# Optimization experiments

Hardware: AMD Instinct MI355X
Metric: run time of the kernel (lower is better)

Reference implementation:

```python
import jax, jax.numpy as jnp
import numpy as np

N = 50000       # nodes
E = 800000      # edges (avg degree 16)
D_IN = 128      # input_dim
H = 256         # hidden_dim
Z = H // 2      # 128, latent / conv3-4 width
D_OUT = 64      # output_dim


def _glorot(key, shape):
    fan_in, fan_out = shape
    lim = float(np.sqrt(6.0 / (fan_in + fan_out)))
    return jax.random.uniform(key, shape, jnp.float32, -lim, lim)


def setup_inputs() -> dict:
    key = jax.random.key(0)
    ks = jax.random.split(key, 16)
    inp = {
        "x": jax.random.uniform(ks[0], (N, D_IN), jnp.float32),
        "edge_index": jax.random.randint(ks[1], (2, E), 0, N, jnp.int32),
        "epsilon": jax.random.normal(ks[2], (N, Z), jnp.float32),
        # SAGEConv params: Wl (neighbor/aggr path, with bias), Wr (root path, no bias)
        "Wl1": _glorot(ks[3], (D_IN, H)), "bl1": jnp.zeros((H,), jnp.float32), "Wr1": _glorot(ks[4], (D_IN, H)),
        "Wl2": _glorot(ks[5], (H, H)),    "bl2": jnp.zeros((H,), jnp.float32), "Wr2": _glorot(ks[6], (H, H)),
        "Wl3": _glorot(ks[7], (Z, Z)),    "bl3": jnp.zeros((Z,), jnp.float32), "Wr3": _glorot(ks[8], (Z, Z)),
        "Wl4": _glorot(ks[9], (Z, Z)),    "bl4": jnp.zeros((Z,), jnp.float32), "Wr4": _glorot(ks[10], (Z, Z)),
        "W_lin": _glorot(ks[11], (Z, D_OUT)), "b_lin": jnp.zeros((D_OUT,), jnp.float32),
    }
    return inp


def _sage_conv(x, src, dst, Wl, bl, Wr):
    # PyG SAGEConv (mean aggr): out = lin_l(mean_{j in N(i)} x_j) + lin_r(x_i)
    msg = x[src]                                             # [E, d] gather
    agg = jax.ops.segment_sum(msg, dst, num_segments=N)      # [N, d]
    cnt = jax.ops.segment_sum(jnp.ones((src.shape[0],), x.dtype), dst, num_segments=N)
    mean = agg / jnp.maximum(cnt, 1.0)[:, None]
    return mean @ Wl + bl + x @ Wr


def reference(x, edge_index, epsilon,
              Wl1, bl1, Wr1, Wl2, bl2, Wr2,
              Wl3, bl3, Wr3, Wl4, bl4, Wr4,
              W_lin, b_lin):
    src, dst = edge_index[0], edge_index[1]
    h = x / 1000.0 - 0.5
    h = jnp.sin(_sage_conv(h, src, dst, Wl1, bl1, Wr1))      # [N, H]
    h = _sage_conv(h, src, dst, Wl2, bl2, Wr2)               # [N, H]
    mean = h[:, :Z]
    log_var = h[:, Z:]
    z = mean + jnp.exp(log_var) * epsilon                    # reparameterize
    h = jax.nn.relu(_sage_conv(z, src, dst, Wl3, bl3, Wr3))
    h = jax.nn.relu(_sage_conv(h, src, dst, Wl4, bl4, Wr4))
    out = jax.nn.sigmoid(h @ W_lin + b_lin) * 1000.0
    return out, mean, log_var
```

## Files before the change

kernel.cpp:

```cpp
#include <hip/hip_runtime.h>
#include <hip/hip_bf16.h>

#define N_NODES 50000
#define E_EDGES 800000

using u16 = unsigned short;
typedef short bf8 __attribute__((ext_vector_type(8)));
typedef float f32x4 __attribute__((ext_vector_type(4)));

__device__ __forceinline__ float bf2f(u16 h) {
    union { unsigned u; float f; } v;
    v.u = ((unsigned)h) << 16;
    return v.f;
}
__device__ __forceinline__ u16 f2bf(float f) {
    union { float f; unsigned u; } v;
    v.f = f;
    unsigned r = v.u + 0x7FFF + ((v.u >> 16) & 1);
    return (u16)(r >> 16);
}

struct WtArgs {
    const float* src[9];
    u16* dst[9];
    int K[9];
    int N[9];
};

__global__ __launch_bounds__(256) void k_wt(WtArgs a) {
    int wi = blockIdx.y;
    int K = a.K[wi], Nn = a.N[wi];
    int tot = K * Nn;
    for (int i = blockIdx.x * 256 + threadIdx.x; i < tot; i += gridDim.x * 256) {
        int n = i / K, k = i % K;
        a.dst[wi][i] = f2bf(a.src[wi][(size_t)k * Nn + n]);
    }
}

__global__ __launch_bounds__(256) void k_prep(const float* __restrict__ x,
                                              u16* __restrict__ h0) {
    int total = N_NODES * 128 / 4;
    for (int i = blockIdx.x * 256 + threadIdx.x; i < total;
         i += gridDim.x * 256) {
        float4 v = *(const float4*)(x + (size_t)i * 4);
        ushort4 o;
        o.x = f2bf(v.x * 0.001f - 0.5f);
        o.y = f2bf(v.y * 0.001f - 0.5f);
        o.z = f2bf(v.z * 0.001f - 0.5f);
        o.w = f2bf(v.w * 0.001f - 0.5f);
        *(ushort4*)(h0 + (size_t)i * 4) = o;
    }
}

__global__ void k_count(const int* __restrict__ dst, int* __restrict__ deg) {
    for (int i = blockIdx.x * blockDim.x + threadIdx.x; i < E_EDGES;
         i += gridDim.x * blockDim.x)
        atomicAdd(&deg[dst[i]], 1);
}

#define SCAN_B 49

__global__ __launch_bounds__(1024) void k_scan1(const int* __restrict__ deg,
                                                int* __restrict__ bsum) {
    __shared__ int sm[1024];
    int i = blockIdx.x * 1024 + threadIdx.x;
    sm[threadIdx.x] = (i < N_NODES) ? deg[i] : 0;
    __syncthreads();
    for (int ofs = 512; ofs > 0; ofs >>= 1) {
        if (threadIdx.x < ofs) sm[threadIdx.x] += sm[threadIdx.x + ofs];
        __syncthreads();
    }
    if (threadIdx.x == 0) bsum[blockIdx.x] = sm[0];
}

__global__ void k_scan2(const int* __restrict__ bsum, int* __restrict__ bofs) {
    int l = threadIdx.x;
    int v = (l < SCAN_B) ? bsum[l] : 0;
    int orig = v;
    for (int d = 1; d < 64; d <<= 1) {
        int u = __shfl_up(v, d, 64);
        if (l >= d) v += u;
    }
    if (l < SCAN_B) bofs[l] = v - orig;
}

__global__ __launch_bounds__(1024) void k_scan3(const int* __restrict__ deg,
                                                const int* __restrict__ bofs,
                                                int* __restrict__ rowptr,
                                                float* __restrict__ dinv) {
    __shared__ int sm[1024];
    int i = blockIdx.x * 1024 + threadIdx.x;
    int d = (i < N_NODES) ? deg[i] : 0;
    sm[threadIdx.x] = d;
    __syncthreads();
    for (int ofs = 1; ofs < 1024; ofs <<= 1) {
        int u = (threadIdx.x >= (unsigned)ofs) ? sm[threadIdx.x - ofs] : 0;
        __syncthreads();
        sm[threadIdx.x] += u;
        __syncthreads();
    }
    if (i < N_NODES) {
        int incl = sm[threadIdx.x] + bofs[blockIdx.x];
        rowptr[i] = incl - d;
        dinv[i] = 1.0f / fmaxf((float)d, 1.0f);
        if (i == N_NODES - 1) rowptr[N_NODES] = incl;
    }
}

__global__ void k_fill(const int* __restrict__ src, const int* __restrict__ dst,
                       const int* __restrict__ rowptr, int* __restrict__ cursor,
                       int* __restrict__ colidx) {
    for (int i = blockIdx.x * blockDim.x + threadIdx.x; i < E_EDGES;
         i += gridDim.x * blockDim.x) {
        int d = dst[i];
        int pos = rowptr[d] + atomicAdd(&cursor[d], 1);
        colidx[pos] = src[i];
    }
}

template <int D>
__global__ __launch_bounds__(256) void k_aggregate(
    const u16* __restrict__ h, const int* __restrict__ rowptr,
    const int* __restrict__ colidx, const float* __restrict__ dinv,
    u16* __restrict__ mean) {
    constexpr int VA = D / 16;
    int node = (int)((blockIdx.x * 256 + threadIdx.x) >> 6);
    int lane = threadIdx.x & 63;
    if (node >= N_NODES) return;
    int sub = lane >> 4, lr = lane & 15;
    int beg = rowptr[node], end = rowptr[node + 1];
    float acc[VA] = {};
    int e = beg + sub;
    for (; e + 4 < end; e += 8) {
        int s0 = colidx[e];
        int s1 = colidx[e + 4];
        const u16* p0 = h + (size_t)s0 * D + lr * VA;
        const u16* p1 = h + (size_t)s1 * D + lr * VA;
        bf8 r0 = *(const bf8*)p0;
        bf8 r1 = *(const bf8*)p1;
        if (VA == 16) {
            bf8 r0b = *(const bf8*)(p0 + 8);
            bf8 r1b = *(const bf8*)(p1 + 8);
#pragma unroll
            for (int j = 0; j < 8; ++j) {
                acc[j] += bf2f((u16)r0[j]) + bf2f((u16)r1[j]);
                acc[8 + j] += bf2f((u16)r0b[j]) + bf2f((u16)r1b[j]);
            }
        } else {
#pragma unroll
            for (int j = 0; j < 8; ++j)
                acc[j] += bf2f((u16)r0[j]) + bf2f((u16)r1[j]);
        }
    }
    for (; e < end; e += 4) {
        int s = colidx[e];
        const u16* row = h + (size_t)s * D + lr * VA;
        bf8 r0 = *(const bf8*)row;
#pragma unroll
        for (int j = 0; j < 8; ++j) acc[j] += bf2f((u16)r0[j]);
        if (VA == 16) {
            bf8 r1 = *(const bf8*)(row + 8);
#pragma unroll
            for (int j = 0; j < 8; ++j) acc[8 + j] += bf2f((u16)r1[j]);
        }
    }
#pragma unroll
    for (int j = 0; j < VA; ++j) {
        acc[j] += __shfl_xor(acc[j], 16);
        acc[j] += __shfl_xor(acc[j], 32);
    }
    if (sub == 0) {
        float inv = dinv[node];
        u16 outv[VA];
#pragma unroll
        for (int j = 0; j < VA; ++j) outv[j] = f2bf(acc[j] * inv);
        u16* o = mean + (size_t)node * D + lr * VA;
        *(bf8*)o = *(bf8*)&outv[0];
        if (VA == 16) *(bf8*)(o + 8) = *(bf8*)&outv[8];
    }
}

enum { ACT_NONE = 0, ACT_SIN = 1, ACT_RELU = 2, ACT_SIGMOID1000 = 3, ACT_VAE = 4 };

template <int K, int NCB, int NC, int ACT, bool OUT_F32, bool TWO_PASS>
__global__ __launch_bounds__(512) void k_gemm(
    const u16* __restrict__ A1, const u16* __restrict__ Wt1,
    const u16* __restrict__ A2, const u16* __restrict__ Wt2,
    const float* __restrict__ bias, void* __restrict__ Cout,
    float* __restrict__ out_mean, float* __restrict__ out_lv,
    const float* __restrict__ eps) {
    constexpr int PK = K + 8;
    constexpr int M = N_NODES;
    constexpr int CH = K / 8;
    constexpr int NG = NCB / 16;
    constexpr int KS = K / 32;
    constexpr int GX = (M / 16 + 7) / 8;
    constexpr int NWG = ((GX + 1) / 2) * 2 * 2;
    constexpr int CPX = NWG / 8;
    extern __shared__ char smem[];
    u16* Bs = (u16*)smem;

    const int bid = blockIdx.x;
    const int wid = (bid & 7) * CPX + (bid >> 3);
    const int x = wid >> 1;
    const int y = wid & 1;
    if (x >= GX) return;

    const int t = threadIdx.x;
    const int lane = t & 63;
    const int wave = t >> 6;
    const int lr = lane & 15;
    const int sub = lane >> 4;
    const int row0 = (x * 8 + wave) * 16;
    const int arow = row0 + lr;
    const bool rowOK = arow < M;

    auto mapRow = [&](int r) {
        if (ACT == ACT_VAE)
            return r < NCB / 2 ? y * (NCB / 2) + r
                               : NC / 2 + y * (NCB / 2) + (r - NCB / 2);
        return y * NCB + r;
    };

    bf8 aF1[KS], aF2[TWO_PASS ? KS : 1];
    {
        const u16* ap = A1 + (size_t)arow * K + sub * 8;
#pragma unroll
        for (int ks = 0; ks < KS; ++ks) {
            bf8 a = {0, 0, 0, 0, 0, 0, 0, 0};
            if (rowOK) a = *(const bf8*)(ap + ks * 32);
            aF1[ks] = a;
        }
    }
    if (TWO_PASS) {
        const u16* ap = A2 + (size_t)arow * K + sub * 8;
#pragma unroll
        for (int ks = 0; ks < KS; ++ks) {
            bf8 a = {0, 0, 0, 0, 0, 0, 0, 0};
            if (rowOK) a = *(const bf8*)(ap + ks * 32);
            aF2[ks] = a;
        }
    }

    f32x4 acc[NG];
#pragma unroll
    for (int i = 0; i < NG; ++i) acc[i] = (f32x4){0.f, 0.f, 0.f, 0.f};

    auto stageW = [&](const u16* __restrict__ Wt) {
#pragma unroll
        for (int i = 0; i < NCB * CH / 512; ++i) {
            int c = t + i * 512;
            int r = c / CH, kc = c % CH;
            *(bf8*)&Bs[r * PK + kc * 8] =
                *(const bf8*)(Wt + (size_t)mapRow(r) * K + kc * 8);
        }
    };
    auto mm = [&](const bf8* aF) {
#pragma unroll
        for (int ks = 0; ks < KS; ++ks) {
#pragma unroll
            for (int ni = 0; ni < NG; ++ni) {
                bf8 b = *(const bf8*)&Bs[(ni * 16 + lr) * PK + ks * 32 + sub * 8];
                acc[ni] =
                    __builtin_amdgcn_mfma_f32_16x16x32_bf16(aF[ks], b, acc[ni],
                                                            0, 0, 0);
            }
        }
    };

    stageW(Wt1);
    __syncthreads();
    mm(aF1);
    if (TWO_PASS) {
        __syncthreads();
        stageW(Wt2);
        __syncthreads();
        mm(aF2);
    }

    if (ACT == ACT_VAE) {
#pragma unroll
        for (int ni = 0; ni < NG / 2; ++ni) {
            int colm = y * (NCB / 2) + ni * 16 + lr;
            float bm = bias[colm];
            float bl = bias[colm + 128];
#pragma unroll
            for (int r = 0; r < 4; ++r) {
                int row = row0 + sub * 4 + r;
                if (row >= M) continue;
                float mv = acc[ni][r] + bm;
                float lv = acc[ni + NG / 2][r] + bl;
                size_t o = (size_t)row * 128 + colm;
                out_mean[o] = mv;
                out_lv[o] = lv;
                ((u16*)Cout)[o] = f2bf(mv + __expf(lv) * eps[o]);
            }
        }
    } else {
#pragma unroll
        for (int ni = 0; ni < NG; ++ni) {
            int col = y * NCB + ni * 16 + lr;
            float bv = bias[col];
#pragma unroll
            for (int r = 0; r < 4; ++r) {
                int row = row0 + sub * 4 + r;
                if (row >= M) continue;
                float v = acc[ni][r] + bv;
                if (ACT == ACT_SIN) v = __sinf(v);
                else if (ACT == ACT_RELU) v = fmaxf(v, 0.f);
                else if (ACT == ACT_SIGMOID1000) v = 1000.f / (1.f + __expf(-v));
                if (OUT_F32)
                    ((float*)Cout)[(size_t)row * NC + col] = v;
                else
                    ((u16*)Cout)[(size_t)row * NC + col] = f2bf(v);
            }
        }
    }
}

extern "C" void kernel_launch(void* const* d_in, const int* in_sizes, int n_in,
                              void* d_out, int out_size, void* d_ws,
                              size_t ws_size, hipStream_t stream) {
    const int N = N_NODES;
    const float* x = (const float*)d_in[0];
    const int* ei = (const int*)d_in[1];
    const float* eps = (const float*)d_in[2];
    const float* Wl1 = (const float*)d_in[3];
    const float* bl1 = (const float*)d_in[4];
    const float* Wr1 = (const float*)d_in[5];
    const float* Wl2 = (const float*)d_in[6];
    const float* bl2 = (const float*)d_in[7];
    const float* Wr2 = (const float*)d_in[8];
    const float* Wl3 = (const float*)d_in[9];
    const float* bl3 = (const float*)d_in[10];
    const float* Wr3 = (const float*)d_in[11];
    const float* Wl4 = (const float*)d_in[12];
    const float* bl4 = (const float*)d_in[13];
    const float* Wr4 = (const float*)d_in[14];
    const float* W_lin = (const float*)d_in[15];
    const float* b_lin = (const float*)d_in[16];

    const int* src = ei;
    const int* dst = ei + E_EDGES;

    char* w = (char*)d_ws;
    auto alloc = [&](size_t b) {
        void* p = (void*)w;
        w += (b + 255) & ~(size_t)255;
        return p;
    };
    int* deg = (int*)alloc((size_t)N * 4);
    int* rowptr = (int*)alloc((size_t)(N + 1) * 4);
    int* cursor = (int*)alloc((size_t)N * 4);
    int* colidx = (int*)alloc((size_t)E_EDGES * 4);
    float* dinv = (float*)alloc((size_t)N * 4);
    int* bsum = (int*)alloc(64 * 4);
    int* bofs = (int*)alloc(64 * 4);
    u16* hbA = (u16*)alloc((size_t)N * 256 * 2);
    u16* hbB = (u16*)alloc((size_t)N * 256 * 2);
    u16* hbC = (u16*)alloc((size_t)N * 256 * 2);
    static const int wK[9] = {128, 128, 256, 256, 128, 128, 128, 128, 128};
    static const int wN[9] = {256, 256, 256, 256, 128, 128, 128, 128, 64};
    u16* Wt[9];
    for (int i = 0; i < 9; ++i) Wt[i] = (u16*)alloc((size_t)wK[i] * wN[i] * 2);

    float* out_final = (float*)d_out;
    float* out_mean = out_final + (size_t)N * 64;
    float* out_lv = out_mean + (size_t)N * 128;

    hipMemsetAsync(deg, 0, (size_t)N * 4, stream);
    hipMemsetAsync(cursor, 0, (size_t)N * 4, stream);

    WtArgs wa;
    const float* wsrc[9] = {Wl1, Wr1, Wl2, Wr2, Wl3, Wr3, Wl4, Wr4, W_lin};
    for (int i = 0; i < 9; ++i) {
        wa.src[i] = wsrc[i];
        wa.dst[i] = Wt[i];
        wa.K[i] = wK[i];
        wa.N[i] = wN[i];
    }
    k_wt<<<dim3(64, 9), 256, 0, stream>>>(wa);

    k_prep<<<2048, 256, 0, stream>>>(x, hbA);
    k_count<<<3125, 256, 0, stream>>>(dst, deg);
    k_scan1<<<SCAN_B, 1024, 0, stream>>>(deg, bsum);
    k_scan2<<<1, 64, 0, stream>>>(bsum, bofs);
    k_scan3<<<SCAN_B, 1024, 0, stream>>>(deg, bofs, rowptr, dinv);
    k_fill<<<3125, 256, 0, stream>>>(src, dst, rowptr, cursor, colidx);

    const int aggBlocks = (N * 64 + 255) / 256;
    const int nwg = 784;
    auto shm = [](int NCB, int K) { return (size_t)NCB * (K + 8) * 2; };

    k_aggregate<128><<<aggBlocks, 256, 0, stream>>>(hbA, rowptr, colidx, dinv,
                                                    hbB);
    k_gemm<128, 128, 256, ACT_SIN, false, true>
        <<<nwg, 512, shm(128, 128), stream>>>(hbB, Wt[0], hbA, Wt[1], bl1, hbC,
                                              nullptr, nullptr, nullptr);

    k_aggregate<256><<<aggBlocks, 256, 0, stream>>>(hbC, rowptr, colidx, dinv,
                                                    hbB);
    k_gemm<256, 128, 256, ACT_VAE, false, true>
        <<<nwg, 512, shm(128, 256), stream>>>(hbB, Wt[2], hbC, Wt[3], bl2, hbA,
                                              out_mean, out_lv, eps);

    k_aggregate<128><<<aggBlocks, 256, 0, stream>>>(hbA, rowptr, colidx, dinv,
                                                    hbB);
    k_gemm<128, 64, 128, ACT_RELU, false, true>
        <<<nwg, 512, shm(64, 128), stream>>>(hbB, Wt[4], hbA, Wt[5], bl3, hbC,
                                             nullptr, nullptr, nullptr);

    k_aggregate<128><<<aggBlocks, 256, 0, stream>>>(hbC, rowptr, colidx, dinv,
                                                    hbB);
    k_gemm<128, 64, 128, ACT_RELU, false, true>
        <<<nwg, 512, shm(64, 128), stream>>>(hbB, Wt[6], hbC, Wt[7], bl4, hbA,
                                             nullptr, nullptr, nullptr);

    k_gemm<128, 32, 64, ACT_SIGMOID1000, true, false>
        <<<nwg, 512, shm(32, 128), stream>>>(hbA, Wt[8], nullptr, nullptr,
                                             b_lin, out_final, nullptr, nullptr,
                                             nullptr);
}
```

Baseline: 381.1 us.

## Pre-pack weights into MFMA fragment order for contiguous LDS staging and reads

Weights are now packed once into the exact per-lane fragment order used by the 16x16x32 bf16 MFMA, so staging into LDS is a straight contiguous copy and each lane reads its B fragment at consecutive addresses. The padded row layout and its index arithmetic are removed, which should reduce LDS bank conflicts and address math in the GEMM. The VAE column-group remapping is expressed at 16-column group granularity. The one-time packing kernel does strided reads of the source weights, but it handles very little data.

```diff
diff --git a/kernel.cpp b/kernel.cpp
--- a/kernel.cpp
+++ b/kernel.cpp
@@ -27,13 +27,23 @@
     int N[9];
 };
 
-__global__ __launch_bounds__(256) void k_wt(WtArgs a) {
+__global__ __launch_bounds__(256) void k_wpack(WtArgs a) {
     int wi = blockIdx.y;
-    int K = a.K[wi], Nn = a.N[wi];
-    int tot = K * Nn;
-    for (int i = blockIdx.x * 256 + threadIdx.x; i < tot; i += gridDim.x * 256) {
-        int n = i / K, k = i % K;
-        a.dst[wi][i] = f2bf(a.src[wi][(size_t)k * Nn + n]);
+    int K = a.K[wi], NC = a.N[wi];
+    int KS = K / 32;
+    int chunks = (NC / 16) * KS * 64;
+    for (int c = blockIdx.x * 256 + threadIdx.x; c < chunks;
+         c += gridDim.x * 256) {
+        int l = c & 63;
+        int rest = c >> 6;
+        int ks = rest % KS, gni = rest / KS;
+        int n = gni * 16 + (l & 15);
+        int kb = ks * 32 + (l >> 4) * 8;
+        u16 outv[8];
+#pragma unroll
+        for (int j = 0; j < 8; ++j)
+            outv[j] = f2bf(a.src[wi][(size_t)(kb + j) * NC + n]);
+        *(bf8*)&a.dst[wi][(size_t)c * 8] = *(bf8*)outv;
     }
 }
 
@@ -184,16 +194,15 @@
 
 template <int K, int NCB, int NC, int ACT, bool OUT_F32, bool TWO_PASS>
 __global__ __launch_bounds__(512) void k_gemm(
-    const u16* __restrict__ A1, const u16* __restrict__ Wt1,
-    const u16* __restrict__ A2, const u16* __restrict__ Wt2,
+    const u16* __restrict__ A1, const u16* __restrict__ Wp1,
+    const u16* __restrict__ A2, const u16* __restrict__ Wp2,
     const float* __restrict__ bias, void* __restrict__ Cout,
     float* __restrict__ out_mean, float* __restrict__ out_lv,
     const float* __restrict__ eps) {
-    constexpr int PK = K + 8;
     constexpr int M = N_NODES;
-    constexpr int CH = K / 8;
     constexpr int NG = NCB / 16;
     constexpr int KS = K / 32;
+    constexpr int CHUNKS = NG * KS * 64;
     constexpr int GX = (M / 16 + 7) / 8;
     constexpr int NWG = ((GX + 1) / 2) * 2 * 2;
     constexpr int CPX = NWG / 8;
@@ -215,11 +224,11 @@
     const int arow = row0 + lr;
     const bool rowOK = arow < M;
 
-    auto mapRow = [&](int r) {
+    auto mapGroup = [&](int ni) {
         if (ACT == ACT_VAE)
-            return r < NCB / 2 ? y * (NCB / 2) + r
-                               : NC / 2 + y * (NCB / 2) + (r - NCB / 2);
-        return y * NCB + r;
+            return ni < NG / 2 ? y * (NG / 2) + ni
+                               : (NC / 32) + y * (NG / 2) + (ni - NG / 2);
+        return y * NG + ni;
     };
 
     bf8 aF1[KS], aF2[TWO_PASS ? KS : 1];
@@ -246,13 +255,15 @@
 #pragma unroll
     for (int i = 0; i < NG; ++i) acc[i] = (f32x4){0.f, 0.f, 0.f, 0.f};
 
-    auto stageW = [&](const u16* __restrict__ Wt) {
-#pragma unroll
-        for (int i = 0; i < NCB * CH / 512; ++i) {
+    auto stageW = [&](const u16* __restrict__ Wp) {
+#pragma unroll
+        for (int i = 0; i < CHUNKS / 512; ++i) {
             int c = t + i * 512;
-            int r = c / CH, kc = c % CH;
-            *(bf8*)&Bs[r * PK + kc * 8] =
-                *(const bf8*)(Wt + (size_t)mapRow(r) * K + kc * 8);
+            int l = c & 63;
+            int ks = (c >> 6) % KS;
+            int ni = c / (64 * KS);
+            size_t gsrc = ((size_t)mapGroup(ni) * KS + ks) * 64 + l;
+            *(bf8*)&Bs[(size_t)c * 8] = *(const bf8*)(Wp + gsrc * 8);
         }
     };
     auto mm = [&](const bf8* aF) {
@@ -260,7 +271,7 @@
         for (int ks = 0; ks < KS; ++ks) {
 #pragma unroll
             for (int ni = 0; ni < NG; ++ni) {
-                bf8 b = *(const bf8*)&Bs[(ni * 16 + lr) * PK + ks * 32 + sub * 8];
+                bf8 b = *(const bf8*)&Bs[(((size_t)ni * KS + ks) * 64 + lane) * 8];
                 acc[ni] =
                     __builtin_amdgcn_mfma_f32_16x16x32_bf16(aF[ks], b, acc[ni],
                                                             0, 0, 0);
@@ -268,12 +279,12 @@
         }
     };
 
-    stageW(Wt1);
+    stageW(Wp1);
     __syncthreads();
     mm(aF1);
     if (TWO_PASS) {
         __syncthreads();
-        stageW(Wt2);
+        stageW(Wp2);
         __syncthreads();
         mm(aF2);
     }
@@ -379,7 +390,7 @@
         wa.K[i] = wK[i];
         wa.N[i] = wN[i];
     }
-    k_wt<<<dim3(64, 9), 256, 0, stream>>>(wa);
+    k_wpack<<<dim3(32, 9), 256, 0, stream>>>(wa);
 
     k_prep<<<2048, 256, 0, stream>>>(x, hbA);
     k_count<<<3125, 256, 0, stream>>>(dst, deg);
@@ -390,7 +401,7 @@
 
     const int aggBlocks = (N * 64 + 255) / 256;
     const int nwg = 784;
-    auto shm = [](int NCB, int K) { return (size_t)NCB * (K + 8) * 2; };
+    auto shm = [](int NCB, int K) { return (size_t)NCB * K * 2; };
 
     k_aggregate<128><<<aggBlocks, 256, 0, stream>>>(hbA, rowptr, colidx, dinv,
                                                     hbB);
```

Result: no change. 379.6 us (-0.4%).
